# Performance work log

Measured on AMD Instinct MI355X. Metric: run time of the kernel, lower is better.

The kernel has to match this reference:

```python
import jax, jax.numpy as jnp
import numpy as np

B, T, I, H, A = 128, 1024, 128, 256, 40


def setup_inputs() -> dict:
    key = jax.random.key(0)
    ks = jax.random.split(key, 10)
    s_ih = 1.0 / np.sqrt(H)
    return {
        "x": jax.random.normal(ks[0], (B, T, I), dtype=jnp.float32),
        "W_ih": jax.random.uniform(ks[1], (3 * H, I), minval=-s_ih, maxval=s_ih, dtype=jnp.float32),
        "W_hh": jax.random.uniform(ks[2], (3 * H, H), minval=-s_ih, maxval=s_ih, dtype=jnp.float32),
        "b_ih": jax.random.uniform(ks[3], (3 * H,), minval=-s_ih, maxval=s_ih, dtype=jnp.float32),
        "b_hh": jax.random.uniform(ks[4], (3 * H,), minval=-s_ih, maxval=s_ih, dtype=jnp.float32),
        "wv_W": jax.random.normal(ks[5], (A, H), dtype=jnp.float32) * 0.05,
        "wv_b": jnp.zeros((A,), dtype=jnp.float32),
        "wu": jax.random.uniform(ks[6], (A,), dtype=jnp.float32),
        "h2o_W": jax.random.normal(ks[7], (1, H), dtype=jnp.float32) * 0.05,
        "h2o_b": jnp.zeros((1,), dtype=jnp.float32),
    }


def _gru_outputs(x, W_ih, W_hh, b_ih, b_hh):
    # Precompute input-side gate projections for all timesteps: [B,T,3H]
    gx = jnp.einsum("bti,gi->btg", x, W_ih) + b_ih
    h0 = jnp.zeros((x.shape[0], H), dtype=x.dtype)

    def step(h, gx_t):
        gh = h @ W_hh.T + b_hh                      # [B,3H]
        xr, xz, xn = jnp.split(gx_t, 3, axis=-1)    # torch gate order r,z,n
        hr, hz, hn = jnp.split(gh, 3, axis=-1)
        r = jax.nn.sigmoid(xr + hr)
        z = jax.nn.sigmoid(xz + hz)
        n = jnp.tanh(xn + r * hn)
        h_new = (1.0 - z) * n + z * h
        return h_new, h_new

    _, hs = jax.lax.scan(step, h0, jnp.swapaxes(gx, 0, 1))  # hs: [T,B,H]
    return jnp.swapaxes(hs, 0, 1)  # [B,T,H]


def reference(x, W_ih, W_hh, b_ih, b_hh, wv_W, wv_b, wu, h2o_W, h2o_b):
    outputs = _gru_outputs(x, W_ih, W_hh, b_ih, b_hh)          # [B,T,H]
    um = jnp.tanh(jnp.einsum("bth,ah->bta", outputs, wv_W) + wv_b)  # [B,T,A]
    alpha = jax.nn.softmax(um @ wu, axis=1)                    # [B,T]
    context = jnp.einsum("bt,bth->bh", alpha, outputs)         # [B,H]
    # dropout_layer is identity in eval mode
    out = context @ h2o_W.T + h2o_b                            # [B,1]
    return out
```

## Files before the change

### kernel.cpp

```cpp
#include <hip/hip_runtime.h>


#define B_ 128
#define T_ 1024
#define I_ 128
#define H_ 256
#define G_ 768
#define A_ 40

typedef _Float16 f16;
typedef _Float16 f16x2 __attribute__((ext_vector_type(2)));
typedef _Float16 f16x8 __attribute__((ext_vector_type(8)));
typedef float    f32x4 __attribute__((ext_vector_type(4)));

__device__ __forceinline__ float fdot2(unsigned a, unsigned b, float c){
#if __has_builtin(__builtin_amdgcn_fdot2)
  return __builtin_amdgcn_fdot2(__builtin_bit_cast(f16x2, a),
                                __builtin_bit_cast(f16x2, b), c, false);
#else
  f16x2 av = __builtin_bit_cast(f16x2, a), bv = __builtin_bit_cast(f16x2, b);
  return c + (float)av.x * (float)bv.x + (float)av.y * (float)bv.y;
#endif
}

__device__ __forceinline__ float2 h2f(unsigned u){
  f16x2 h = __builtin_bit_cast(f16x2, u);
  return make_float2((float)h.x, (float)h.y);
}
__device__ __forceinline__ unsigned f2h2(float a, float b){
  f16x2 h; h.x = (f16)a; h.y = (f16)b;
  return __builtin_bit_cast(unsigned, h);
}
__device__ __forceinline__ float sigm_(float x){ return 1.f / (1.f + __expf(-x)); }
__device__ __forceinline__ float tanh_(float x){ return 1.f - 2.f / (__expf(2.f * x) + 1.f); }

__device__ __forceinline__ float xor1_sum(float x){
  int xi = __builtin_bit_cast(int, x);
  int sw = __builtin_amdgcn_update_dpp(0, xi, 0xB1, 0xF, 0xF, true);
  return x + __builtin_bit_cast(float, sw);
}

__global__ __launch_bounds__(256) void k_prep_w(const float* __restrict__ W,
                                                unsigned* __restrict__ Wp){
  int idx = blockIdx.x * 256 + threadIdx.x;
  int dd  = idx >> 9;
  int col = idx & 511;
  int c = dd >> 6, d = dd & 63;
  int g = col >> 1, sub = col & 1;
  int r = c * 256 + g;
  int k = sub * 128 + 2 * d;
  Wp[(size_t)dd * 512 + col] = f2h2(W[r * 256 + k], W[r * 256 + k + 1]);
}

__global__ __launch_bounds__(256) void k_gx(const float* __restrict__ x,
                                            const float* __restrict__ wih,
                                            const float* __restrict__ bih,
                                            const float* __restrict__ bhh,
                                            f16* __restrict__ gx){
  __shared__ __align__(16) f16 XA[128 * 128];
  __shared__ __align__(16) f16 XB[64 * 128];
  const int tid = threadIdx.x;
  const int m0 = blockIdx.x * 128, n0 = blockIdx.y * 64;

  #pragma unroll
  for (int u = 0; u < 16; ++u){
    int idx = tid + 256 * u;
    int row = idx >> 5, k4 = idx & 31;
    float4 v = *(const float4*)(x + (size_t)(m0 + row) * I_ + k4 * 4);
    unsigned byte = (unsigned)(row * 256 + k4 * 8) ^ ((row & 7) << 4);
    *(uint2*)((char*)XA + byte) = make_uint2(f2h2(v.x, v.y), f2h2(v.z, v.w));
  }
  #pragma unroll
  for (int u = 0; u < 8; ++u){
    int idx = tid + 256 * u;
    int row = idx >> 5, k4 = idx & 31;
    float4 v = *(const float4*)(wih + (size_t)(n0 + row) * I_ + k4 * 4);
    unsigned byte = (unsigned)(row * 256 + k4 * 8) ^ ((row & 7) << 4);
    *(uint2*)((char*)XB + byte) = make_uint2(f2h2(v.x, v.y), f2h2(v.z, v.w));
  }
  __syncthreads();

  const int l = tid & 63, w = tid >> 6;
  const int q = l >> 4, m16 = l & 15;
  f32x4 acc[2][4];
  #pragma unroll
  for (int i = 0; i < 2; ++i)
    #pragma unroll
    for (int nt = 0; nt < 4; ++nt) acc[i][nt] = (f32x4){0.f, 0.f, 0.f, 0.f};

  #pragma unroll
  for (int kt = 0; kt < 4; ++kt){
    f16x8 af[2];
    #pragma unroll
    for (int i = 0; i < 2; ++i){
      int row = (2 * w + i) * 16 + m16;
      unsigned byte = (unsigned)(row * 256 + kt * 64 + q * 16) ^ ((row & 7) << 4);
      af[i] = *(const f16x8*)((const char*)XA + byte);
    }
    #pragma unroll
    for (int nt = 0; nt < 4; ++nt){
      int row = nt * 16 + m16;
      unsigned byte = (unsigned)(row * 256 + kt * 64 + q * 16) ^ ((row & 7) << 4);
      f16x8 bv = *(const f16x8*)((const char*)XB + byte);
      acc[0][nt] = __builtin_amdgcn_mfma_f32_16x16x32_f16(af[0], bv, acc[0][nt], 0, 0, 0);
      acc[1][nt] = __builtin_amdgcn_mfma_f32_16x16x32_f16(af[1], bv, acc[1][nt], 0, 0, 0);
    }
  }

  float bn[4];
  #pragma unroll
  for (int nt = 0; nt < 4; ++nt){
    int n = n0 + nt * 16 + m16;
    bn[nt] = bih[n] + (n < 512 ? bhh[n] : 0.f);
  }

  __syncthreads();
  f16* ST = XA;
  #pragma unroll
  for (int i = 0; i < 2; ++i)
    #pragma unroll
    for (int nt = 0; nt < 4; ++nt)
      #pragma unroll
      for (int j = 0; j < 4; ++j){
        int row = (2 * w + i) * 16 + 4 * q + j;
        ST[row * 72 + nt * 16 + m16] = (f16)(acc[i][nt][j] + bn[nt]);
      }
  __syncthreads();
  #pragma unroll
  for (int u = 0; u < 4; ++u){
    int idx = tid + 256 * u;
    int row = idx >> 3, c = idx & 7;
    uint4 v = *(const uint4*)(ST + row * 72 + c * 8);
    *(uint4*)(gx + (size_t)(m0 + row) * G_ + n0 + c * 8) = v;
  }
}

__global__ __launch_bounds__(512, 2) void k_gru(const unsigned* __restrict__ Wp,
                                                unsigned* __restrict__ gx,
                                                const float* __restrict__ bhh){
  __shared__ uint4 hb[2][36];
  const int tid = threadIdx.x;
  const int g = tid >> 1, sub = tid & 1;
  const int b = blockIdx.x;

  unsigned w0[64], w1[64], w2[64];
  #pragma unroll
  for (int d = 0; d < 64; ++d) w0[d] = Wp[(size_t)(d      ) * 512 + tid];
  #pragma unroll
  for (int d = 0; d < 64; ++d) w1[d] = Wp[(size_t)(64  + d) * 512 + tid];
  #pragma unroll
  for (int d = 0; d < 64; ++d) w2[d] = Wp[(size_t)(128 + d) * 512 + tid];

  const float bn_ = bhh[512 + g];
  float hprev = 0.f;
  if (tid < 36) hb[0][tid] = make_uint4(0, 0, 0, 0);

  f16* gxp = (f16*)gx + (size_t)b * T_ * G_;
  float xr = 0.f, xz = 0.f, xn = 0.f;
  if (sub == 0){ xr = (float)gxp[g]; xz = (float)gxp[H_ + g]; xn = (float)gxp[2 * H_ + g]; }
  __syncthreads();

  const int rb = sub * 18;
  int cur = 0;
  for (int t = 0; t < T_; ++t){
    float pr = 0.f, pz = 0.f, pn = 0.f;
    if (sub == 0 && t + 1 < T_){
      const f16* nx = gxp + (size_t)(t + 1) * G_;
      pr = (float)nx[g]; pz = (float)nx[H_ + g]; pn = (float)nx[2 * H_ + g];
    }

    float a00 = 0.f, a01 = 0.f, a10 = 0.f, a11 = 0.f, a20 = 0.f, a21 = 0.f;
    #pragma unroll
    for (int i = 0; i < 16; ++i){
      uint4 hv = hb[cur][rb + i];
      a00 = fdot2(w0[4*i+0], hv.x, a00); a01 = fdot2(w0[4*i+1], hv.y, a01);
      a00 = fdot2(w0[4*i+2], hv.z, a00); a01 = fdot2(w0[4*i+3], hv.w, a01);
      a10 = fdot2(w1[4*i+0], hv.x, a10); a11 = fdot2(w1[4*i+1], hv.y, a11);
      a10 = fdot2(w1[4*i+2], hv.z, a10); a11 = fdot2(w1[4*i+3], hv.w, a11);
      a20 = fdot2(w2[4*i+0], hv.x, a20); a21 = fdot2(w2[4*i+1], hv.y, a21);
      a20 = fdot2(w2[4*i+2], hv.z, a20); a21 = fdot2(w2[4*i+3], hv.w, a21);
    }
    float ar = xor1_sum(a00 + a01);
    float az = xor1_sum(a10 + a11);
    float an = xor1_sum(a20 + a21);

    if (sub == 0){
      float rg = sigm_(xr + ar);
      float zg = sigm_(xz + az);
      float ng = tanh_(xn + rg * (an + bn_));
      float h  = (1.f - zg) * ng + zg * hprev;
      hprev = h;
      f16 hh = (f16)h;
      ((f16*)hb[cur ^ 1])[g + (g >> 7) * 16] = hh;
      gxp[(size_t)t * G_ + g] = hh;
      xr = pr; xz = pz; xn = pn;
    }
    __syncthreads();
    cur ^= 1;
  }
}

__global__ __launch_bounds__(256) void k_score(const f16* __restrict__ outs,
                                               const float* __restrict__ wvW,
                                               const float* __restrict__ wvb,
                                               const float* __restrict__ wu,
                                               float* __restrict__ s){
  __shared__ uint4 OT[32 * 33];
  __shared__ float WV[A_ * 260];
  const int tid = threadIdx.x;
  const int m0 = blockIdx.x * 32;

  #pragma unroll
  for (int u = 0; u < 4; ++u){
    int idx = tid + 256 * u;
    int row = idx >> 5, col = idx & 31;
    OT[row * 33 + col] = *(const uint4*)(outs + (size_t)(m0 + row) * G_ + col * 8);
  }
  #pragma unroll
  for (int u = 0; u < 10; ++u){
    int f = tid + 256 * u;
    int a = f >> 6, k4 = f & 63;
    float4 v = *(const float4*)(wvW + a * 256 + k4 * 4);
    *(float4*)(WV + a * 260 + k4 * 4) = v;
  }
  __syncthreads();

  const int m = tid >> 3, aq = tid & 7;
  float acc[5] = {0.f, 0.f, 0.f, 0.f, 0.f};
  for (int i = 0; i < 32; ++i){
    uint4 oc = OT[m * 33 + i];
    float2 o01 = h2f(oc.x), o23 = h2f(oc.y), o45 = h2f(oc.z), o67 = h2f(oc.w);
    #pragma unroll
    for (int sa = 0; sa < 5; ++sa){
      int a = aq + sa * 8;
      const float* wr = &WV[a * 260 + i * 8];
      float4 w0 = *(const float4*)wr;
      float4 w1 = *(const float4*)(wr + 4);
      acc[sa] += o01.x*w0.x + o01.y*w0.y + o23.x*w0.z + o23.y*w0.w
               + o45.x*w1.x + o45.y*w1.y + o67.x*w1.z + o67.y*w1.w;
    }
  }
  float sp = 0.f;
  #pragma unroll
  for (int sa = 0; sa < 5; ++sa){
    int a = aq + sa * 8;
    sp += wu[a] * tanh_(acc[sa] + wvb[a]);
  }
  sp += __shfl_xor(sp, 1);
  sp += __shfl_xor(sp, 2);
  sp += __shfl_xor(sp, 4);
  if (aq == 0) s[m0 + m] = sp;
}

__global__ __launch_bounds__(256) void k_ctx(const f16* __restrict__ outs,
                                             const float* __restrict__ s,
                                             const float* __restrict__ h2oW,
                                             const float* __restrict__ h2ob,
                                             float* __restrict__ out){
  __shared__ float AL[T_];
  __shared__ float red[8];
  const int tid = threadIdx.x;
  const int b = blockIdx.x;
  const float* sb = s + (size_t)b * T_;

  float v0 = sb[tid], v1 = sb[tid + 256], v2 = sb[tid + 512], v3 = sb[tid + 768];
  float mx = fmaxf(fmaxf(v0, v1), fmaxf(v2, v3));
  #pragma unroll
  for (int msk = 1; msk < 64; msk <<= 1) mx = fmaxf(mx, __shfl_xor(mx, msk));
  if ((tid & 63) == 0) red[tid >> 6] = mx;
  __syncthreads();
  mx = fmaxf(fmaxf(red[0], red[1]), fmaxf(red[2], red[3]));

  float e0 = __expf(v0 - mx), e1 = __expf(v1 - mx), e2 = __expf(v2 - mx), e3 = __expf(v3 - mx);
  float zs = e0 + e1 + e2 + e3;
  #pragma unroll
  for (int msk = 1; msk < 64; msk <<= 1) zs += __shfl_xor(zs, msk);
  if ((tid & 63) == 0) red[4 + (tid >> 6)] = zs;
  __syncthreads();
  float invZ = 1.f / (red[4] + red[5] + red[6] + red[7]);
  AL[tid] = e0 * invZ; AL[tid + 256] = e1 * invZ;
  AL[tid + 512] = e2 * invZ; AL[tid + 768] = e3 * invZ;
  __syncthreads();

  const f16* ob = outs + (size_t)b * T_ * G_;
  float acc = 0.f;
  for (int t = 0; t < T_; t += 4){
    acc += AL[t + 0] * (float)ob[(size_t)(t + 0) * G_ + tid];
    acc += AL[t + 1] * (float)ob[(size_t)(t + 1) * G_ + tid];
    acc += AL[t + 2] * (float)ob[(size_t)(t + 2) * G_ + tid];
    acc += AL[t + 3] * (float)ob[(size_t)(t + 3) * G_ + tid];
  }
  __syncthreads();
  float val = acc * h2oW[tid];
  #pragma unroll
  for (int msk = 1; msk < 64; msk <<= 1) val += __shfl_xor(val, msk);
  if ((tid & 63) == 0) red[tid >> 6] = val;
  __syncthreads();
  if (tid == 0) out[b] = red[0] + red[1] + red[2] + red[3] + h2ob[0];
}

extern "C" void kernel_launch(void* const* d_in, const int* in_sizes, int n_in,
                              void* d_out, int out_size, void* d_ws, size_t ws_size,
                              hipStream_t stream){
  const float* x    = (const float*)d_in[0];
  const float* wih  = (const float*)d_in[1];
  const float* whh  = (const float*)d_in[2];
  const float* bih  = (const float*)d_in[3];
  const float* bhh  = (const float*)d_in[4];
  const float* wvW  = (const float*)d_in[5];
  const float* wvb  = (const float*)d_in[6];
  const float* wu   = (const float*)d_in[7];
  const float* h2oW = (const float*)d_in[8];
  const float* h2ob = (const float*)d_in[9];
  float* out = (float*)d_out;

  char* ws = (char*)d_ws;
  float*    s  = (float*)ws;
  unsigned* Wp = (unsigned*)(ws + 524288);
  unsigned* gx = (unsigned*)(ws + 917504);

  k_prep_w<<<384, 256, 0, stream>>>(whh, Wp);
  k_gx<<<dim3((B_ * T_) / 128, G_ / 64), 256, 0, stream>>>(x, wih, bih, bhh, (f16*)gx);
  k_gru<<<B_, 512, 0, stream>>>(Wp, gx, bhh);
  k_score<<<(B_ * T_) / 32, 256, 0, stream>>>((const f16*)gx, wvW, wvb, wu, s);
  k_ctx<<<B_, 256, 0, stream>>>((const f16*)gx, s, h2oW, h2ob, out);
}
```

Before: 1.708 ms.

## Split GRU hidden-unit dot products across four lanes instead of two

The recurrent GRU kernel now uses 1024 threads per batch row, with four lanes per hidden unit each covering a quarter of the K dimension, and reduces them with a two-step DPP quad sum. This halves the per-thread serial fdot2 chain and the register-resident weight slices on the latency-bound timestep loop. Every lane now computes the gate math redundantly, and only lane 0 writes h. The price is a larger workgroup, so each timestep barrier has to synchronise more waves, plus an extra DPP step per gate.

```diff
diff --git a/kernel.cpp b/kernel.cpp
--- a/kernel.cpp
+++ b/kernel.cpp
@@ -34,22 +34,25 @@
 __device__ __forceinline__ float sigm_(float x){ return 1.f / (1.f + __expf(-x)); }
 __device__ __forceinline__ float tanh_(float x){ return 1.f - 2.f / (__expf(2.f * x) + 1.f); }
 
-__device__ __forceinline__ float xor1_sum(float x){
-  int xi = __builtin_bit_cast(int, x);
-  int sw = __builtin_amdgcn_update_dpp(0, xi, 0xB1, 0xF, 0xF, true);
-  return x + __builtin_bit_cast(float, sw);
+__device__ __forceinline__ float quad_sum(float x){
+  int t = __builtin_amdgcn_update_dpp(0, __builtin_bit_cast(int, x),
+                                      0xB1, 0xF, 0xF, true);
+  x += __builtin_bit_cast(float, t);
+  t = __builtin_amdgcn_update_dpp(0, __builtin_bit_cast(int, x),
+                                  0x4E, 0xF, 0xF, true);
+  return x + __builtin_bit_cast(float, t);
 }
 
 __global__ __launch_bounds__(256) void k_prep_w(const float* __restrict__ W,
                                                 unsigned* __restrict__ Wp){
   int idx = blockIdx.x * 256 + threadIdx.x;
-  int dd  = idx >> 9;
-  int col = idx & 511;
-  int c = dd >> 6, d = dd & 63;
-  int g = col >> 1, sub = col & 1;
+  int dd  = idx >> 10;
+  int col = idx & 1023;
+  int c = dd >> 5, d = dd & 31;
+  int g = col >> 2, qs = col & 3;
   int r = c * 256 + g;
-  int k = sub * 128 + 2 * d;
-  Wp[(size_t)dd * 512 + col] = f2h2(W[r * 256 + k], W[r * 256 + k + 1]);
+  int k = qs * 64 + 2 * d;
+  Wp[(size_t)dd * 1024 + col] = f2h2(W[r * 256 + k], W[r * 256 + k + 1]);
 }
 
 __global__ __launch_bounds__(256) void k_gx(const float* __restrict__ x,
@@ -135,66 +138,64 @@
   }
 }
 
-__global__ __launch_bounds__(512, 2) void k_gru(const unsigned* __restrict__ Wp,
-                                                unsigned* __restrict__ gx,
-                                                const float* __restrict__ bhh){
-  __shared__ uint4 hb[2][36];
+__global__ __launch_bounds__(1024, 4) void k_gru(const unsigned* __restrict__ Wp,
+                                                 unsigned* __restrict__ gx,
+                                                 const float* __restrict__ bhh){
+  __shared__ uint4 hb[2][4][9];
   const int tid = threadIdx.x;
-  const int g = tid >> 1, sub = tid & 1;
+  const int g = tid >> 2, qs = tid & 3;
   const int b = blockIdx.x;
 
-  unsigned w0[64], w1[64], w2[64];
-  #pragma unroll
-  for (int d = 0; d < 64; ++d) w0[d] = Wp[(size_t)(d      ) * 512 + tid];
-  #pragma unroll
-  for (int d = 0; d < 64; ++d) w1[d] = Wp[(size_t)(64  + d) * 512 + tid];
-  #pragma unroll
-  for (int d = 0; d < 64; ++d) w2[d] = Wp[(size_t)(128 + d) * 512 + tid];
+  unsigned w0[32], w1[32], w2[32];
+  #pragma unroll
+  for (int d = 0; d < 32; ++d) w0[d] = Wp[(size_t)(d     ) * 1024 + tid];
+  #pragma unroll
+  for (int d = 0; d < 32; ++d) w1[d] = Wp[(size_t)(32 + d) * 1024 + tid];
+  #pragma unroll
+  for (int d = 0; d < 32; ++d) w2[d] = Wp[(size_t)(64 + d) * 1024 + tid];
 
   const float bn_ = bhh[512 + g];
   float hprev = 0.f;
-  if (tid < 36) hb[0][tid] = make_uint4(0, 0, 0, 0);
+  if (tid < 72) ((uint4*)hb)[tid] = make_uint4(0, 0, 0, 0);
 
   f16* gxp = (f16*)gx + (size_t)b * T_ * G_;
-  float xr = 0.f, xz = 0.f, xn = 0.f;
-  if (sub == 0){ xr = (float)gxp[g]; xz = (float)gxp[H_ + g]; xn = (float)gxp[2 * H_ + g]; }
-  __syncthreads();
-
-  const int rb = sub * 18;
+  float xr = (float)gxp[g], xz = (float)gxp[H_ + g], xn = (float)gxp[2 * H_ + g];
+  __syncthreads();
+
   int cur = 0;
   for (int t = 0; t < T_; ++t){
     float pr = 0.f, pz = 0.f, pn = 0.f;
-    if (sub == 0 && t + 1 < T_){
+    if (t + 1 < T_){
       const f16* nx = gxp + (size_t)(t + 1) * G_;
       pr = (float)nx[g]; pz = (float)nx[H_ + g]; pn = (float)nx[2 * H_ + g];
     }
 
-    float a00 = 0.f, a01 = 0.f, a10 = 0.f, a11 = 0.f, a20 = 0.f, a21 = 0.f;
-    #pragma unroll
-    for (int i = 0; i < 16; ++i){
-      uint4 hv = hb[cur][rb + i];
-      a00 = fdot2(w0[4*i+0], hv.x, a00); a01 = fdot2(w0[4*i+1], hv.y, a01);
-      a00 = fdot2(w0[4*i+2], hv.z, a00); a01 = fdot2(w0[4*i+3], hv.w, a01);
-      a10 = fdot2(w1[4*i+0], hv.x, a10); a11 = fdot2(w1[4*i+1], hv.y, a11);
-      a10 = fdot2(w1[4*i+2], hv.z, a10); a11 = fdot2(w1[4*i+3], hv.w, a11);
-      a20 = fdot2(w2[4*i+0], hv.x, a20); a21 = fdot2(w2[4*i+1], hv.y, a21);
-      a20 = fdot2(w2[4*i+2], hv.z, a20); a21 = fdot2(w2[4*i+3], hv.w, a21);
-    }
-    float ar = xor1_sum(a00 + a01);
-    float az = xor1_sum(a10 + a11);
-    float an = xor1_sum(a20 + a21);
-
-    if (sub == 0){
-      float rg = sigm_(xr + ar);
-      float zg = sigm_(xz + az);
-      float ng = tanh_(xn + rg * (an + bn_));
-      float h  = (1.f - zg) * ng + zg * hprev;
-      hprev = h;
+    float a0 = 0.f, b0 = 0.f, a1 = 0.f, b1 = 0.f, a2 = 0.f, b2 = 0.f;
+    #pragma unroll
+    for (int i = 0; i < 8; ++i){
+      uint4 hv = hb[cur][qs][i];
+      a0 = fdot2(w0[4*i+0], hv.x, a0); b0 = fdot2(w0[4*i+1], hv.y, b0);
+      a0 = fdot2(w0[4*i+2], hv.z, a0); b0 = fdot2(w0[4*i+3], hv.w, b0);
+      a1 = fdot2(w1[4*i+0], hv.x, a1); b1 = fdot2(w1[4*i+1], hv.y, b1);
+      a1 = fdot2(w1[4*i+2], hv.z, a1); b1 = fdot2(w1[4*i+3], hv.w, b1);
+      a2 = fdot2(w2[4*i+0], hv.x, a2); b2 = fdot2(w2[4*i+1], hv.y, b2);
+      a2 = fdot2(w2[4*i+2], hv.z, a2); b2 = fdot2(w2[4*i+3], hv.w, b2);
+    }
+    float ar = quad_sum(a0 + b0);
+    float az = quad_sum(a1 + b1);
+    float an = quad_sum(a2 + b2);
+
+    float rg = sigm_(xr + ar);
+    float zg = sigm_(xz + az);
+    float ng = tanh_(xn + rg * (an + bn_));
+    float h  = (1.f - zg) * ng + zg * hprev;
+    hprev = h;
+    if (qs == 0){
       f16 hh = (f16)h;
-      ((f16*)hb[cur ^ 1])[g + (g >> 7) * 16] = hh;
+      ((f16*)&hb[cur ^ 1][g >> 6][0])[g & 63] = hh;
       gxp[(size_t)t * G_ + g] = hh;
-      xr = pr; xz = pz; xn = pn;
-    }
+    }
+    xr = pr; xz = pz; xn = pn;
     __syncthreads();
     cur ^= 1;
   }
@@ -321,7 +322,7 @@
 
   k_prep_w<<<384, 256, 0, stream>>>(whh, Wp);
   k_gx<<<dim3((B_ * T_) / 128, G_ / 64), 256, 0, stream>>>(x, wih, bih, bhh, (f16*)gx);
-  k_gru<<<B_, 512, 0, stream>>>(Wp, gx, bhh);
+  k_gru<<<B_, 1024, 0, stream>>>(Wp, gx, bhh);
   k_score<<<(B_ * T_) / 32, 256, 0, stream>>>((const f16*)gx, wvW, wvb, wu, s);
   k_ctx<<<B_, 256, 0, stream>>>((const f16*)gx, s, h2oW, h2ob, out);
 }
```

New measurement: 1.734 ms. About the same (+1.5%).

## Process two batch rows per GRU block to reuse register-resident weights

Applied to the files above, without the earlier changes.

Each k_gru block now runs the recurrence for two batch rows at once, so every register-held W_hh weight is used for two dot products per load from LDS. Half as many blocks launch. The change also adds a two-step-ahead prefetch of the gx inputs, computes the gates on both lanes of each pair, uses a hardware reciprocal in sigmoid and tanh, and replaces __syncthreads with a raw barrier after an explicit LDS wait. The cost is a longer serial chain per step and only 64 blocks on the device, which leaves many CUs idle.

```diff
diff --git a/kernel.cpp b/kernel.cpp
--- a/kernel.cpp
+++ b/kernel.cpp
@@ -31,13 +31,14 @@
   f16x2 h; h.x = (f16)a; h.y = (f16)b;
   return __builtin_bit_cast(unsigned, h);
 }
-__device__ __forceinline__ float sigm_(float x){ return 1.f / (1.f + __expf(-x)); }
-__device__ __forceinline__ float tanh_(float x){ return 1.f - 2.f / (__expf(2.f * x) + 1.f); }
-
-__device__ __forceinline__ float xor1_sum(float x){
-  int xi = __builtin_bit_cast(int, x);
-  int sw = __builtin_amdgcn_update_dpp(0, xi, 0xB1, 0xF, 0xF, true);
-  return x + __builtin_bit_cast(float, sw);
+__device__ __forceinline__ float rcp_(float x){ return __builtin_amdgcn_rcpf(x); }
+__device__ __forceinline__ float sigm_(float x){ return rcp_(1.f + __expf(-x)); }
+__device__ __forceinline__ float tanh_(float x){ return 1.f - 2.f * rcp_(__expf(2.f * x) + 1.f); }
+
+__device__ __forceinline__ float xs(float x){
+  int t = __builtin_amdgcn_update_dpp(0, __builtin_bit_cast(int, x),
+                                      0xB1, 0xF, 0xF, true);
+  return x + __builtin_bit_cast(float, t);
 }
 
 __global__ __launch_bounds__(256) void k_prep_w(const float* __restrict__ W,
@@ -135,13 +136,15 @@
   }
 }
 
-__global__ __launch_bounds__(512, 2) void k_gru(const unsigned* __restrict__ Wp,
-                                                unsigned* __restrict__ gx,
-                                                const float* __restrict__ bhh){
-  __shared__ uint4 hb[2][36];
+__global__ __launch_bounds__(512)
+__attribute__((amdgpu_waves_per_eu(2, 2)))
+void k_gru(const unsigned* __restrict__ Wp,
+           unsigned* __restrict__ gx,
+           const float* __restrict__ bhh){
+  __shared__ uint4 hb[2][2][36];
   const int tid = threadIdx.x;
   const int g = tid >> 1, sub = tid & 1;
-  const int b = blockIdx.x;
+  const int b0 = blockIdx.x * 2;
 
   unsigned w0[64], w1[64], w2[64];
   #pragma unroll
@@ -152,50 +155,71 @@
   for (int d = 0; d < 64; ++d) w2[d] = Wp[(size_t)(128 + d) * 512 + tid];
 
   const float bn_ = bhh[512 + g];
-  float hprev = 0.f;
-  if (tid < 36) hb[0][tid] = make_uint4(0, 0, 0, 0);
-
-  f16* gxp = (f16*)gx + (size_t)b * T_ * G_;
-  float xr = 0.f, xz = 0.f, xn = 0.f;
-  if (sub == 0){ xr = (float)gxp[g]; xz = (float)gxp[H_ + g]; xn = (float)gxp[2 * H_ + g]; }
-  __syncthreads();
-
-  const int rb = sub * 18;
+  float hpA = 0.f, hpB = 0.f;
+  if (tid < 72) ((uint4*)hb)[tid] = make_uint4(0, 0, 0, 0);
+
+  f16* gxA = (f16*)gx + (size_t)(b0    ) * T_ * G_;
+  f16* gxB = (f16*)gx + (size_t)(b0 + 1) * T_ * G_;
+
+  f16 ar0 = gxA[g],      az0 = gxA[H_+g],      an0 = gxA[2*H_+g];
+  f16 ar1 = gxA[G_+g],   az1 = gxA[G_+H_+g],   an1 = gxA[G_+2*H_+g];
+  f16 br0 = gxB[g],      bz0 = gxB[H_+g],      bn0 = gxB[2*H_+g];
+  f16 br1 = gxB[G_+g],   bz1 = gxB[G_+H_+g],   bn1 = gxB[G_+2*H_+g];
+  __syncthreads();
+
   int cur = 0;
   for (int t = 0; t < T_; ++t){
-    float pr = 0.f, pz = 0.f, pn = 0.f;
-    if (sub == 0 && t + 1 < T_){
-      const f16* nx = gxp + (size_t)(t + 1) * G_;
-      pr = (float)nx[g]; pz = (float)nx[H_ + g]; pn = (float)nx[2 * H_ + g];
-    }
-
-    float a00 = 0.f, a01 = 0.f, a10 = 0.f, a11 = 0.f, a20 = 0.f, a21 = 0.f;
+    const f16* nxA = gxA + (size_t)((t + 2) & (T_ - 1)) * G_;
+    const f16* nxB = gxB + (size_t)((t + 2) & (T_ - 1)) * G_;
+    f16 ar2 = nxA[g], az2 = nxA[H_+g], an2 = nxA[2*H_+g];
+    f16 br2 = nxB[g], bz2 = nxB[H_+g], bn2 = nxB[2*H_+g];
+
+    const uint4* hA = &hb[cur][0][sub * 18];
+    const uint4* hB = &hb[cur][1][sub * 18];
+    float aA0=0,bA0=0,aA1=0,bA1=0,aA2=0,bA2=0;
+    float aB0=0,bB0=0,aB1=0,bB1=0,aB2=0,bB2=0;
     #pragma unroll
     for (int i = 0; i < 16; ++i){
-      uint4 hv = hb[cur][rb + i];
-      a00 = fdot2(w0[4*i+0], hv.x, a00); a01 = fdot2(w0[4*i+1], hv.y, a01);
-      a00 = fdot2(w0[4*i+2], hv.z, a00); a01 = fdot2(w0[4*i+3], hv.w, a01);
-      a10 = fdot2(w1[4*i+0], hv.x, a10); a11 = fdot2(w1[4*i+1], hv.y, a11);
-      a10 = fdot2(w1[4*i+2], hv.z, a10); a11 = fdot2(w1[4*i+3], hv.w, a11);
-      a20 = fdot2(w2[4*i+0], hv.x, a20); a21 = fdot2(w2[4*i+1], hv.y, a21);
-      a20 = fdot2(w2[4*i+2], hv.z, a20); a21 = fdot2(w2[4*i+3], hv.w, a21);
-    }
-    float ar = xor1_sum(a00 + a01);
-    float az = xor1_sum(a10 + a11);
-    float an = xor1_sum(a20 + a21);
+      uint4 hvA = hA[i];
+      uint4 hvB = hB[i];
+      aA0=fdot2(w0[4*i+0],hvA.x,aA0); bA0=fdot2(w0[4*i+1],hvA.y,bA0);
+      aA0=fdot2(w0[4*i+2],hvA.z,aA0); bA0=fdot2(w0[4*i+3],hvA.w,bA0);
+      aB0=fdot2(w0[4*i+0],hvB.x,aB0); bB0=fdot2(w0[4*i+1],hvB.y,bB0);
+      aB0=fdot2(w0[4*i+2],hvB.z,aB0); bB0=fdot2(w0[4*i+3],hvB.w,bB0);
+      aA1=fdot2(w1[4*i+0],hvA.x,aA1); bA1=fdot2(w1[4*i+1],hvA.y,bA1);
+      aA1=fdot2(w1[4*i+2],hvA.z,aA1); bA1=fdot2(w1[4*i+3],hvA.w,bA1);
+      aB1=fdot2(w1[4*i+0],hvB.x,aB1); bB1=fdot2(w1[4*i+1],hvB.y,bB1);
+      aB1=fdot2(w1[4*i+2],hvB.z,aB1); bB1=fdot2(w1[4*i+3],hvB.w,bB1);
+      aA2=fdot2(w2[4*i+0],hvA.x,aA2); bA2=fdot2(w2[4*i+1],hvA.y,bA2);
+      aA2=fdot2(w2[4*i+2],hvA.z,aA2); bA2=fdot2(w2[4*i+3],hvA.w,bA2);
+      aB2=fdot2(w2[4*i+0],hvB.x,aB2); bB2=fdot2(w2[4*i+1],hvB.y,bB2);
+      aB2=fdot2(w2[4*i+2],hvB.z,aB2); bB2=fdot2(w2[4*i+3],hvB.w,bB2);
+    }
+    float sAr = xs(aA0 + bA0), sAz = xs(aA1 + bA1), sAn = xs(aA2 + bA2);
+    float sBr = xs(aB0 + bB0), sBz = xs(aB1 + bB1), sBn = xs(aB2 + bB2);
+
+    float rA = sigm_((float)ar0 + sAr);
+    float zA = sigm_((float)az0 + sAz);
+    float nA = tanh_((float)an0 + rA * (sAn + bn_));
+    float hAv = (1.f - zA) * nA + zA * hpA;  hpA = hAv;
+    float rB = sigm_((float)br0 + sBr);
+    float zB = sigm_((float)bz0 + sBz);
+    float nB = tanh_((float)bn0 + rB * (sBn + bn_));
+    float hBv = (1.f - zB) * nB + zB * hpB;  hpB = hBv;
 
     if (sub == 0){
-      float rg = sigm_(xr + ar);
-      float zg = sigm_(xz + az);
-      float ng = tanh_(xn + rg * (an + bn_));
-      float h  = (1.f - zg) * ng + zg * hprev;
-      hprev = h;
-      f16 hh = (f16)h;
-      ((f16*)hb[cur ^ 1])[g + (g >> 7) * 16] = hh;
-      gxp[(size_t)t * G_ + g] = hh;
-      xr = pr; xz = pz; xn = pn;
-    }
-    __syncthreads();
+      f16 ha = (f16)hAv, hbv = (f16)hBv;
+      ((f16*)&hb[cur ^ 1][0][0])[g + (g >> 7) * 16] = ha;
+      ((f16*)&hb[cur ^ 1][1][0])[g + (g >> 7) * 16] = hbv;
+      gxA[(size_t)t * G_ + g] = ha;
+      gxB[(size_t)t * G_ + g] = hbv;
+    }
+    ar0 = ar1; az0 = az1; an0 = an1;  ar1 = ar2; az1 = az2; an1 = an2;
+    br0 = br1; bz0 = bz1; bn0 = bn1;  br1 = br2; bz1 = bz2; bn1 = bn2;
+
+    asm volatile("s_waitcnt lgkmcnt(0)" ::: "memory");
+    __builtin_amdgcn_s_barrier();
+    asm volatile("" ::: "memory");
     cur ^= 1;
   }
 }
@@ -321,7 +345,7 @@
 
   k_prep_w<<<384, 256, 0, stream>>>(whh, Wp);
   k_gx<<<dim3((B_ * T_) / 128, G_ / 64), 256, 0, stream>>>(x, wih, bih, bhh, (f16*)gx);
-  k_gru<<<B_, 512, 0, stream>>>(Wp, gx, bhh);
+  k_gru<<<B_ / 2, 512, 0, stream>>>(Wp, gx, bhh);
   k_score<<<(B_ * T_) / 32, 256, 0, stream>>>((const f16*)gx, wvW, wvb, wu, s);
   k_ctx<<<B_, 256, 0, stream>>>((const f16*)gx, s, h2oW, h2ob, out);
 }
```

Result: slower. 2.353 ms (+37.7%).
